# Optimization experiments

Measured on AMD Instinct MI355X. Metric: run time of the kernel, lower is better.

The kernel has to match this reference:

```python
import jax, jax.numpy as jnp
import numpy as np

TEMP = 0.07
BATCH, DIM, NUM_ATTRS = 8192, 512, 4
NUM_PROTOS = 2 ** NUM_ATTRS  # all binary combos present => unique() size is static


def setup_inputs() -> dict:
    key = jax.random.key(0)
    z_flowed = jax.random.normal(key, (BATCH, DIM), dtype=jnp.float32)
    # binary attribute combos, all 16 present; first column = MSB (matches torch.unique row sort)
    combo = jnp.arange(BATCH, dtype=jnp.int32) % NUM_PROTOS
    shifts = jnp.arange(NUM_ATTRS - 1, -1, -1, dtype=jnp.int32)
    attributes = ((combo[:, None] >> shifts[None, :]) & 1).astype(jnp.float32)
    return {"z_flowed": z_flowed, "attributes": attributes}


def _l2norm(x, axis=-1, eps=1e-12):
    n = jnp.sqrt(jnp.sum(x * x, axis=axis, keepdims=True))
    return x / jnp.maximum(n, eps)  # F.normalize semantics


def reference(z_flowed, attributes):
    B, D = z_flowed.shape
    num_attrs = attributes.shape[1]
    P = 2 ** num_attrs
    z_norm = _l2norm(z_flowed, axis=1)

    # inverse indices of torch.unique(attributes, dim=0): binary row -> code (MSB = col 0)
    shifts = jnp.arange(num_attrs - 1, -1, -1)
    inverse = jnp.sum((attributes > 0.5).astype(jnp.int32) * (1 << shifts)[None, :], axis=1)

    # prototype = normalized segment-mean of z_norm per attribute combo (detached)
    sums = jax.ops.segment_sum(z_norm, inverse, num_segments=P)          # [P, D]
    counts = jax.ops.segment_sum(jnp.ones((B,), z_norm.dtype), inverse, num_segments=P)
    means = sums / jnp.maximum(counts, 1.0)[:, None]
    prototypes = jax.lax.stop_gradient(_l2norm(means, axis=1))
    prototypes = jnp.where(counts[:, None] > 0, prototypes, 0.0)

    # prototype contrastive term
    proto_sim = (z_norm @ prototypes.T) / TEMP                            # [B, P]
    exp_sim = jnp.exp(proto_sim)
    pos = exp_sim[jnp.arange(B), inverse]
    alls = jnp.maximum(jnp.sum(exp_sim, axis=1), 1e-8)
    loss = -jnp.mean(jnp.log(pos / alls + 1e-8))

    # pairwise term (positives only when BOTH attribute rows are all-ones)
    pairwise = (z_norm @ z_norm.T) / TEMP                                 # [B, B]
    attr_sim = attributes @ attributes.T
    pos_mask = (attr_sim == num_attrs).astype(z_norm.dtype)
    pos_mask = pos_mask * (1.0 - jnp.eye(B, dtype=z_norm.dtype))
    exp_pw = jnp.exp(pairwise)
    pos_sims = jnp.sum(exp_pw * pos_mask, axis=1)
    all_sims = jnp.sum(exp_pw, axis=1) - jnp.diagonal(exp_pw)
    valid = jnp.sum(pos_mask, axis=1) > 0
    per_row = -jnp.log(pos_sims / (all_sims + 1e-8) + 1e-8)
    n_valid = jnp.sum(valid.astype(z_norm.dtype))
    pairwise_loss = jnp.sum(jnp.where(valid, per_row, 0.0)) / jnp.maximum(n_valid, 1.0)
    loss = jnp.where(n_valid > 0, 0.7 * loss + 0.3 * pairwise_loss, loss)
    return loss
```

## Files before the change

kernel.cpp:

```cpp
#include <hip/hip_runtime.h>
#include <math.h>

#define NB 8192
#define ND 512
#define NPROTO 16
#define NBLK 256
#define TINV 14.285714285714286f
#define PW_BLOCKS 256
#define PL_BLOCKS 256

typedef short short8 __attribute__((ext_vector_type(8)));
typedef float float4v __attribute__((ext_vector_type(4)));

__device__ __forceinline__ unsigned short f2bf(float f) {
  unsigned u = __builtin_bit_cast(unsigned, f);
  unsigned r = (u + 0x7FFFu + ((u >> 16) & 1u)) >> 16;
  return (unsigned short)r;
}
__device__ __forceinline__ float bflo(unsigned u) {
  return __builtin_bit_cast(float, u << 16);
}
__device__ __forceinline__ float bfhi(unsigned u) {
  return __builtin_bit_cast(float, u & 0xFFFF0000u);
}

__global__ __launch_bounds__(512) void k_norm(
    const float* __restrict__ z, const float* __restrict__ attr,
    unsigned short* __restrict__ znb, float* __restrict__ partialSum,
    int* __restrict__ code)
{
  __shared__ float acc[NPROTO * ND];
  const int t = threadIdx.x, lane = t & 63, wid = t >> 6;
  for (int i = t; i < NPROTO * ND; i += 512) acc[i] = 0.f;
  __syncthreads();
  #pragma unroll
  for (int rr = 0; rr < 4; ++rr) {
    const int r = blockIdx.x * 32 + wid * 4 + rr;
    const float* zr = z + (size_t)r * ND;
    float v[8];
    #pragma unroll
    for (int jj = 0; jj < 8; ++jj) v[jj] = zr[lane + jj * 64];
    float s = 0.f;
    #pragma unroll
    for (int jj = 0; jj < 8; ++jj) s += v[jj] * v[jj];
    #pragma unroll
    for (int o = 32; o > 0; o >>= 1) s += __shfl_xor(s, o);
    const float inv = 1.f / fmaxf(sqrtf(s), 1e-12f);
    const float* a = attr + (size_t)r * 4;
    const int c = (a[0] > 0.5f ? 8 : 0) | (a[1] > 0.5f ? 4 : 0) |
                  (a[2] > 0.5f ? 2 : 0) | (a[3] > 0.5f ? 1 : 0);
    float* accRow = acc + c * ND;
    #pragma unroll
    for (int jj = 0; jj < 8; ++jj) {
      const float zv = v[jj] * inv;
      atomicAdd(&accRow[lane + jj * 64], zv);
      znb[(size_t)r * ND + lane + jj * 64] = f2bf(zv);
    }
    if (lane == 0) code[r] = c;
  }
  __syncthreads();
  for (int i = t; i < NPROTO * ND; i += 512) {
    const int p = i >> 9, d = i & 511;
    partialSum[(size_t)((p << 8) | blockIdx.x) * ND + d] = acc[i];
  }
}

__global__ __launch_bounds__(256) void k_reduce1(
    const float* __restrict__ partialSum, float* __restrict__ partial2)
{
  const int t = threadIdx.x;
  const int p = blockIdx.x >> 4, c = blockIdx.x & 15;
  const float* base = partialSum + (size_t)(p * NBLK + c * 16) * ND;
  float s0 = 0.f, s1 = 0.f;
  #pragma unroll
  for (int k = 0; k < 16; ++k) {
    s0 += base[k * ND + t];
    s1 += base[k * ND + t + 256];
  }
  partial2[(size_t)(p * 16 + c) * ND + t] = s0;
  partial2[(size_t)(p * 16 + c) * ND + t + 256] = s1;
}

__global__ __launch_bounds__(512) void k_protonorm(
    const float* __restrict__ partial2, const int* __restrict__ code,
    float* __restrict__ protos, int* __restrict__ validList,
    int* __restrict__ validCnt)
{
  __shared__ float red[8];
  __shared__ int lcnt;
  const int t = threadIdx.x, lane = t & 63, wid = t >> 6;
  const int p = blockIdx.x;
  if (t == 0) lcnt = 0;
  __syncthreads();
  const float* base = partial2 + (size_t)p * 16 * ND;
  float s = 0.f;
  #pragma unroll
  for (int c = 0; c < 16; ++c)
    s += base[c * ND + t];
  float cl = 0.f;
  for (int r = t; r < NB; r += 512) {
    const int match = (code[r] == p) ? 1 : 0;
    cl += (float)match;
    if (p == NPROTO - 1 && match) {
      const int slot = atomicAdd(&lcnt, 1);
      validList[slot] = r;
    }
  }
  #pragma unroll
  for (int o = 32; o > 0; o >>= 1) cl += __shfl_xor(cl, o);
  if (lane == 0) red[wid] = cl;
  __syncthreads();
  const float cTot = red[0]+red[1]+red[2]+red[3]+red[4]+red[5]+red[6]+red[7];
  __syncthreads();
  const float mean = s / fmaxf(cTot, 1.f);
  float sq = mean * mean;
  #pragma unroll
  for (int o = 32; o > 0; o >>= 1) sq += __shfl_xor(sq, o);
  if (lane == 0) red[wid] = sq;
  __syncthreads();
  const float sum = red[0]+red[1]+red[2]+red[3]+red[4]+red[5]+red[6]+red[7];
  const float scale = (cTot > 0.f) ? 1.f / fmaxf(sqrtf(sum), 1e-12f) : 0.f;
  protos[p * ND + t] = mean * scale;
  if (p == NPROTO - 1 && t == 0) validCnt[0] = lcnt;
}

#define PLD (ND + 4)
#define SMEM_BYTES 41472
__global__ __launch_bounds__(512) void k_main(
    const unsigned short* __restrict__ znb, const float* __restrict__ protos,
    const int* __restrict__ code, const int* __restrict__ validList,
    const int* __restrict__ validCnt,
    float* __restrict__ partialAll, float* __restrict__ partialPos,
    float* __restrict__ plPart)
{
  __shared__ __align__(16) char smem[SMEM_BYTES];
  __shared__ float red3[8];
  const int t = threadIdx.x, lane = t & 63, wid = t >> 6;
  const int bi = blockIdx.x;
  if (bi < PW_BLOCKS) {
    unsigned short* aT = (unsigned short*)smem;
    unsigned short* bT = aT + 64 * 64;
    int* rowIdx = (int*)(bT + 256 * 64);
    unsigned char* aoSh = (unsigned char*)(rowIdx + 64);
    const int wv = wid >> 2, ww = wid & 3;
    const int m = validCnt[0];
    const int nIT = (m + 63) >> 6;
    const int items = nIT * 32;
    const int grp = lane >> 4, cl = lane & 15;
    for (int wi = bi; wi < items; wi += PW_BLOCKS) {
      const int i0 = (wi >> 5) * 64;
      const int jt = wi & 31;
      const int jb = jt * 256;
      __syncthreads();
      if (t < 64) rowIdx[t] = (i0 + t < m) ? validList[i0 + t] : -1;
      if (t < 256) aoSh[t] = (code[jb + t] == NPROTO - 1) ? 1 : 0;
      float4v acc[2][4];
      #pragma unroll
      for (int mi = 0; mi < 2; ++mi)
        #pragma unroll
        for (int nj = 0; nj < 4; ++nj) acc[mi][nj] = (float4v)(0.f);
      for (int kc = 0; kc < 8; ++kc) {
        const int k0 = kc * 64;
        __syncthreads();
        {
          const int ia = t >> 3, kq = t & 7;
          const int ri = rowIdx[ia];
          const int srow = (ri < 0) ? 0 : ri;
          const uint4 v = *(const uint4*)(znb + (size_t)srow * ND + k0 + kq * 8);
          *(uint4*)((char*)aT + ia * 128 + ((kq * 16) ^ ((ia & 7) << 4))) = v;
        }
        #pragma unroll
        for (int h = 0; h < 4; ++h) {
          const int f = t + h * 512;
          const int j = f >> 3, kq = f & 7;
          const uint4 v = *(const uint4*)(znb + (size_t)(jb + j) * ND + k0 + kq * 8);
          *(uint4*)((char*)bT + j * 128 + ((kq * 16) ^ ((j & 7) << 4))) = v;
        }
        __syncthreads();
        #pragma unroll
        for (int ks = 0; ks < 2; ++ks) {
          const int kb = ks * 64 + grp * 16;
          short8 af[2], bf[4];
          #pragma unroll
          for (int mi = 0; mi < 2; ++mi) {
            const int rw = wv * 32 + mi * 16 + cl;
            af[mi] = *(const short8*)((char*)aT + rw * 128 + (kb ^ ((rw & 7) << 4)));
          }
          #pragma unroll
          for (int nj = 0; nj < 4; ++nj) {
            const int rw = ww * 64 + nj * 16 + cl;
            bf[nj] = *(const short8*)((char*)bT + rw * 128 + (kb ^ ((rw & 7) << 4)));
          }
          #pragma unroll
          for (int mi = 0; mi < 2; ++mi)
            #pragma unroll
            for (int nj = 0; nj < 4; ++nj)
              acc[mi][nj] = __builtin_amdgcn_mfma_f32_16x16x32_bf16(af[mi], bf[nj], acc[mi][nj], 0, 0, 0);
        }
      }
      #pragma unroll
      for (int mi = 0; mi < 2; ++mi) {
        float sA[4] = {0.f, 0.f, 0.f, 0.f}, sP[4] = {0.f, 0.f, 0.f, 0.f};
        int ri[4];
        #pragma unroll
        for (int q = 0; q < 4; ++q) ri[q] = rowIdx[wv * 32 + mi * 16 + grp * 4 + q];
        #pragma unroll
        for (int nj = 0; nj < 4; ++nj) {
          const int jl = ww * 64 + nj * 16 + cl;
          const int jg = jb + jl;
          const float ao = aoSh[jl] ? 1.f : 0.f;
          #pragma unroll
          for (int q = 0; q < 4; ++q) {
            float e = __expf(acc[mi][nj][q] * TINV);
            e = (jg == ri[q]) ? 0.f : e;
            sA[q] += e;
            sP[q] += e * ao;
          }
        }
        #pragma unroll
        for (int q = 0; q < 4; ++q) {
          #pragma unroll
          for (int o = 1; o < 16; o <<= 1) {
            sA[q] += __shfl_xor(sA[q], o);
            sP[q] += __shfl_xor(sP[q], o);
          }
        }
        if (cl == 0) {
          const int slot0 = i0 + wv * 32 + mi * 16 + grp * 4;
          const int jt2 = jt * 4 + ww;
          if (slot0 + 3 < m) {
            *(float4*)&partialAll[(size_t)jt2 * NB + slot0] =
                make_float4(sA[0], sA[1], sA[2], sA[3]);
            *(float4*)&partialPos[(size_t)jt2 * NB + slot0] =
                make_float4(sP[0], sP[1], sP[2], sP[3]);
          } else {
            #pragma unroll
            for (int q = 0; q < 4; ++q) {
              if (slot0 + q < m) {
                partialAll[(size_t)jt2 * NB + slot0 + q] = sA[q];
                partialPos[(size_t)jt2 * NB + slot0 + q] = sP[q];
              }
            }
          }
        }
      }
    }
  } else {
    float* pl = (float*)smem;
    const int pb = bi - PW_BLOCKS;
    for (int i = t; i < NPROTO * ND; i += 512)
      pl[(i >> 9) * PLD + (i & 511)] = protos[i];
    __syncthreads();
    const int p = lane & 15, grp = lane >> 4;
    float lacc = 0.f;
    #pragma unroll
    for (int rr = 0; rr < 4; ++rr) {
      const int r = pb * 32 + wid * 4 + rr;
      const uint4* zr = (const uint4*)(znb + (size_t)r * ND + grp * 128);
      const float* pbp = &pl[p * PLD + grp * 128];
      float s = 0.f;
      #pragma unroll
      for (int it = 0; it < 16; ++it) {
        const uint4 u = zr[it];
        const float4 p0 = *(const float4*)(pbp + it * 8);
        const float4 p1 = *(const float4*)(pbp + it * 8 + 4);
        s += bflo(u.x)*p0.x + bfhi(u.x)*p0.y + bflo(u.y)*p0.z + bfhi(u.y)*p0.w;
        s += bflo(u.z)*p1.x + bfhi(u.z)*p1.y + bflo(u.w)*p1.z + bfhi(u.w)*p1.w;
      }
      s += __shfl_xor(s, 16);
      s += __shfl_xor(s, 32);
      const float e = __expf(s * TINV);
      float alls = e;
      alls += __shfl_xor(alls, 1);
      alls += __shfl_xor(alls, 2);
      alls += __shfl_xor(alls, 4);
      alls += __shfl_xor(alls, 8);
      const int c = code[r];
      const float pos = __shfl(e, (lane & ~15) | c);
      if (lane == 0) lacc += -logf(pos / fmaxf(alls, 1e-8f) + 1e-8f);
    }
    if (lane == 0) red3[wid] = lacc;
    __syncthreads();
    if (t == 0)
      plPart[pb] = red3[0]+red3[1]+red3[2]+red3[3]+red3[4]+red3[5]+red3[6]+red3[7];
  }
}

__global__ __launch_bounds__(1024) void k_final(
    const float* __restrict__ partialAll, const float* __restrict__ partialPos,
    const float* __restrict__ plPart, const int* __restrict__ validCnt,
    float* __restrict__ out)
{
  __shared__ float shA[1024], shP[1024];
  __shared__ float red[16], red2[16];
  const int t = threadIdx.x, lane = t & 63, wid = t >> 6;
  const int m = validCnt[0];
  const int nvalid = (m >= 2) ? m : 0;
  const int slot = t & 511, half = t >> 9;
  float sa = 0.f, sp = 0.f;
  if (slot < nvalid) {
    const int k0 = half * 64;
    #pragma unroll 8
    for (int k = k0; k < k0 + 64; ++k) {
      sa += partialAll[(size_t)k * NB + slot];
      sp += partialPos[(size_t)k * NB + slot];
    }
  }
  shA[t] = sa; shP[t] = sp;
  __syncthreads();
  float s = 0.f;
  if (t < 512 && slot < nvalid) {
    const float A = shA[t] + shA[t + 512];
    const float P = shP[t] + shP[t + 512];
    s = -logf(P / (A + 1e-8f) + 1e-8f);
  }
  float pls = (t < PL_BLOCKS) ? plPart[t] : 0.f;
  #pragma unroll
  for (int o = 32; o > 0; o >>= 1) {
    s += __shfl_xor(s, o);
    pls += __shfl_xor(pls, o);
  }
  if (lane == 0) { red[wid] = s; red2[wid] = pls; }
  __syncthreads();
  if (t == 0) {
    float total = 0.f, plTot = 0.f;
    #pragma unroll
    for (int w = 0; w < 16; ++w) { total += red[w]; plTot += red2[w]; }
    const float proto = plTot / (float)NB;
    float loss = proto;
    if (nvalid > 0) loss = 0.7f * proto + 0.3f * (total / (float)nvalid);
    out[0] = loss;
  }
}

extern "C" void kernel_launch(void* const* d_in, const int* in_sizes, int n_in,
                              void* d_out, int out_size, void* d_ws, size_t ws_size,
                              hipStream_t stream) {
  const float* z = (const float*)d_in[0];
  const float* attr = (const float*)d_in[1];
  unsigned short* znb = (unsigned short*)d_ws;
  float* partialSum = (float*)(znb + (size_t)NB * ND);
  float* partialAll = partialSum;
  float* partialPos = partialSum + (size_t)128 * NB;
  char* w = (char*)(partialSum + (size_t)NBLK * NPROTO * ND);
  float* partial2 = (float*)w;      w += (size_t)NPROTO * 16 * ND * 4;
  int* validCnt = (int*)w;          w += 16;
  int* code = (int*)w;              w += NB * 4;
  int* validList = (int*)w;         w += NB * 4;
  float* protos = (float*)w;        w += NPROTO * ND * 4;
  float* plPart = (float*)w;        w += PL_BLOCKS * 4;
  k_norm<<<dim3(NBLK), dim3(512), 0, stream>>>(z, attr, znb, partialSum, code);
  k_reduce1<<<dim3(256), dim3(256), 0, stream>>>(partialSum, partial2);
  k_protonorm<<<dim3(NPROTO), dim3(512), 0, stream>>>(partial2, code, protos,
                                                      validList, validCnt);
  k_main<<<dim3(PW_BLOCKS + PL_BLOCKS), dim3(512), 0, stream>>>(
      znb, protos, code, validList, validCnt, partialAll, partialPos, plPart);
  k_final<<<dim3(1), dim3(1024), 0, stream>>>(partialAll, partialPos, plPart,
                                              validCnt, (float*)d_out);
}
```

Baseline: 68.66 us.

## Double-buffer pairwise GEMM tiles using direct global-to-LDS loads

Result: slower. 73.40 us (+6.9%).

```diff
diff --git a/kernel.cpp b/kernel.cpp
--- a/kernel.cpp
+++ b/kernel.cpp
@@ -22,6 +22,11 @@
 }
 __device__ __forceinline__ float bfhi(unsigned u) {
   return __builtin_bit_cast(float, u & 0xFFFF0000u);
+}
+__device__ __forceinline__ void gld16(const unsigned short* g, unsigned short* l) {
+  __builtin_amdgcn_global_load_lds(
+      (const __attribute__((address_space(1))) void*)g,
+      (__attribute__((address_space(3))) void*)l, 16, 0, 0);
 }
 
 __global__ __launch_bounds__(512) void k_norm(
@@ -125,7 +130,7 @@
 }
 
 #define PLD (ND + 4)
-#define SMEM_BYTES 41472
+#define SMEM_BYTES 81920
 __global__ __launch_bounds__(512) void k_main(
     const unsigned short* __restrict__ znb, const float* __restrict__ protos,
     const int* __restrict__ code, const int* __restrict__ validList,
@@ -138,45 +143,57 @@
   const int t = threadIdx.x, lane = t & 63, wid = t >> 6;
   const int bi = blockIdx.x;
   if (bi < PW_BLOCKS) {
-    unsigned short* aT = (unsigned short*)smem;
-    unsigned short* bT = aT + 64 * 64;
-    int* rowIdx = (int*)(bT + 256 * 64);
-    unsigned char* aoSh = (unsigned char*)(rowIdx + 64);
+    char* const Abuf[2] = { smem, smem + 8192 };
+    char* const Bbuf[2] = { smem + 16384, smem + 49152 };
     const int wv = wid >> 2, ww = wid & 3;
     const int m = validCnt[0];
     const int nIT = (m + 63) >> 6;
     const int items = nIT * 32;
     const int grp = lane >> 4, cl = lane & 15;
+    const int iaA = t >> 3;
+    const int kqA = (t & 7) ^ (iaA & 7);
     for (int wi = bi; wi < items; wi += PW_BLOCKS) {
       const int i0 = (wi >> 5) * 64;
       const int jt = wi & 31;
       const int jb = jt * 256;
-      __syncthreads();
-      if (t < 64) rowIdx[t] = (i0 + t < m) ? validList[i0 + t] : -1;
-      if (t < 256) aoSh[t] = (code[jb + t] == NPROTO - 1) ? 1 : 0;
+      const int slotA = i0 + iaA;
+      const int srowA = (slotA < m) ? validList[slotA] : 0;
+      {
+        gld16(znb + (size_t)srowA * ND + kqA * 8,
+              (unsigned short*)(Abuf[0] + wid * 1024));
+        #pragma unroll
+        for (int h = 0; h < 4; ++h) {
+          const int ci = h * 512 + t;
+          const int j = ci >> 3;
+          const int kq = (t & 7) ^ (j & 7);
+          gld16(znb + (size_t)(jb + j) * ND + kq * 8,
+                (unsigned short*)(Bbuf[0] + h * 8192 + wid * 1024));
+        }
+      }
       float4v acc[2][4];
       #pragma unroll
       for (int mi = 0; mi < 2; ++mi)
         #pragma unroll
         for (int nj = 0; nj < 4; ++nj) acc[mi][nj] = (float4v)(0.f);
+      int cur = 0;
+      #pragma unroll
       for (int kc = 0; kc < 8; ++kc) {
-        const int k0 = kc * 64;
         __syncthreads();
-        {
-          const int ia = t >> 3, kq = t & 7;
-          const int ri = rowIdx[ia];
-          const int srow = (ri < 0) ? 0 : ri;
-          const uint4 v = *(const uint4*)(znb + (size_t)srow * ND + k0 + kq * 8);
-          *(uint4*)((char*)aT + ia * 128 + ((kq * 16) ^ ((ia & 7) << 4))) = v;
-        }
-        #pragma unroll
-        for (int h = 0; h < 4; ++h) {
-          const int f = t + h * 512;
-          const int j = f >> 3, kq = f & 7;
-          const uint4 v = *(const uint4*)(znb + (size_t)(jb + j) * ND + k0 + kq * 8);
-          *(uint4*)((char*)bT + j * 128 + ((kq * 16) ^ ((j & 7) << 4))) = v;
-        }
-        __syncthreads();
+        if (kc < 7) {
+          const int k0 = (kc + 1) * 64;
+          gld16(znb + (size_t)srowA * ND + k0 + kqA * 8,
+                (unsigned short*)(Abuf[cur ^ 1] + wid * 1024));
+          #pragma unroll
+          for (int h = 0; h < 4; ++h) {
+            const int ci = h * 512 + t;
+            const int j = ci >> 3;
+            const int kq = (t & 7) ^ (j & 7);
+            gld16(znb + (size_t)(jb + j) * ND + k0 + kq * 8,
+                  (unsigned short*)(Bbuf[cur ^ 1] + h * 8192 + wid * 1024));
+          }
+        }
+        const char* aC = Abuf[cur];
+        const char* bC = Bbuf[cur];
         #pragma unroll
         for (int ks = 0; ks < 2; ++ks) {
           const int kb = ks * 64 + grp * 16;
@@ -184,12 +201,12 @@
           #pragma unroll
           for (int mi = 0; mi < 2; ++mi) {
             const int rw = wv * 32 + mi * 16 + cl;
-            af[mi] = *(const short8*)((char*)aT + rw * 128 + (kb ^ ((rw & 7) << 4)));
+            af[mi] = *(const short8*)(aC + rw * 128 + (kb ^ ((rw & 7) << 4)));
           }
           #pragma unroll
           for (int nj = 0; nj < 4; ++nj) {
             const int rw = ww * 64 + nj * 16 + cl;
-            bf[nj] = *(const short8*)((char*)bT + rw * 128 + (kb ^ ((rw & 7) << 4)));
+            bf[nj] = *(const short8*)(bC + rw * 128 + (kb ^ ((rw & 7) << 4)));
           }
           #pragma unroll
           for (int mi = 0; mi < 2; ++mi)
@@ -197,18 +214,22 @@
             for (int nj = 0; nj < 4; ++nj)
               acc[mi][nj] = __builtin_amdgcn_mfma_f32_16x16x32_bf16(af[mi], bf[nj], acc[mi][nj], 0, 0, 0);
         }
+        cur ^= 1;
       }
       #pragma unroll
       for (int mi = 0; mi < 2; ++mi) {
         float sA[4] = {0.f, 0.f, 0.f, 0.f}, sP[4] = {0.f, 0.f, 0.f, 0.f};
         int ri[4];
         #pragma unroll
-        for (int q = 0; q < 4; ++q) ri[q] = rowIdx[wv * 32 + mi * 16 + grp * 4 + q];
+        for (int q = 0; q < 4; ++q) {
+          const int sl = i0 + wv * 32 + mi * 16 + grp * 4 + q;
+          ri[q] = (sl < m) ? validList[sl] : -1;
+        }
         #pragma unroll
         for (int nj = 0; nj < 4; ++nj) {
           const int jl = ww * 64 + nj * 16 + cl;
           const int jg = jb + jl;
-          const float ao = aoSh[jl] ? 1.f : 0.f;
+          const float ao = (code[jg] == NPROTO - 1) ? 1.f : 0.f;
           #pragma unroll
           for (int q = 0; q < 4; ++q) {
             float e = __expf(acc[mi][nj][q] * TINV);
```

## Merge prototype reduction into atomics and fold normalization into main kernel

Applied to the files above, without the earlier changes.

After: 72.05 us. 4.9% more time.

```diff
diff --git a/kernel.cpp b/kernel.cpp
--- a/kernel.cpp
+++ b/kernel.cpp
@@ -27,11 +27,13 @@
 __global__ __launch_bounds__(512) void k_norm(
     const float* __restrict__ z, const float* __restrict__ attr,
     unsigned short* __restrict__ znb, float* __restrict__ partialSum,
-    int* __restrict__ code)
+    int* __restrict__ code, float* __restrict__ protoSumG)
 {
   __shared__ float acc[NPROTO * ND];
   const int t = threadIdx.x, lane = t & 63, wid = t >> 6;
   for (int i = t; i < NPROTO * ND; i += 512) acc[i] = 0.f;
+  if (blockIdx.x == 0)
+    for (int i = t; i < NPROTO * ND; i += 512) protoSumG[i] = 0.f;
   __syncthreads();
   #pragma unroll
   for (int rr = 0; rr < 4; ++rr) {
@@ -66,68 +68,41 @@
 }
 
 __global__ __launch_bounds__(256) void k_reduce1(
-    const float* __restrict__ partialSum, float* __restrict__ partial2)
+    const float* __restrict__ partialSum, const int* __restrict__ code,
+    float* __restrict__ protoSumG, int* __restrict__ validList,
+    int* __restrict__ validCnt)
 {
   const int t = threadIdx.x;
-  const int p = blockIdx.x >> 4, c = blockIdx.x & 15;
-  const float* base = partialSum + (size_t)(p * NBLK + c * 16) * ND;
-  float s0 = 0.f, s1 = 0.f;
-  #pragma unroll
-  for (int k = 0; k < 16; ++k) {
-    s0 += base[k * ND + t];
-    s1 += base[k * ND + t + 256];
-  }
-  partial2[(size_t)(p * 16 + c) * ND + t] = s0;
-  partial2[(size_t)(p * 16 + c) * ND + t + 256] = s1;
-}
-
-__global__ __launch_bounds__(512) void k_protonorm(
-    const float* __restrict__ partial2, const int* __restrict__ code,
-    float* __restrict__ protos, int* __restrict__ validList,
-    int* __restrict__ validCnt)
-{
-  __shared__ float red[8];
-  __shared__ int lcnt;
-  const int t = threadIdx.x, lane = t & 63, wid = t >> 6;
-  const int p = blockIdx.x;
-  if (t == 0) lcnt = 0;
-  __syncthreads();
-  const float* base = partial2 + (size_t)p * 16 * ND;
-  float s = 0.f;
-  #pragma unroll
-  for (int c = 0; c < 16; ++c)
-    s += base[c * ND + t];
-  float cl = 0.f;
-  for (int r = t; r < NB; r += 512) {
-    const int match = (code[r] == p) ? 1 : 0;
-    cl += (float)match;
-    if (p == NPROTO - 1 && match) {
-      const int slot = atomicAdd(&lcnt, 1);
-      validList[slot] = r;
-    }
-  }
-  #pragma unroll
-  for (int o = 32; o > 0; o >>= 1) cl += __shfl_xor(cl, o);
-  if (lane == 0) red[wid] = cl;
-  __syncthreads();
-  const float cTot = red[0]+red[1]+red[2]+red[3]+red[4]+red[5]+red[6]+red[7];
-  __syncthreads();
-  const float mean = s / fmaxf(cTot, 1.f);
-  float sq = mean * mean;
-  #pragma unroll
-  for (int o = 32; o > 0; o >>= 1) sq += __shfl_xor(sq, o);
-  if (lane == 0) red[wid] = sq;
-  __syncthreads();
-  const float sum = red[0]+red[1]+red[2]+red[3]+red[4]+red[5]+red[6]+red[7];
-  const float scale = (cTot > 0.f) ? 1.f / fmaxf(sqrtf(sum), 1e-12f) : 0.f;
-  protos[p * ND + t] = mean * scale;
-  if (p == NPROTO - 1 && t == 0) validCnt[0] = lcnt;
+  if (blockIdx.x < 256) {
+    const int p = blockIdx.x >> 4, c = blockIdx.x & 15;
+    const float* base = partialSum + (size_t)(p * NBLK + c * 16) * ND;
+    float s0 = 0.f, s1 = 0.f;
+    #pragma unroll
+    for (int k = 0; k < 16; ++k) {
+      s0 += base[k * ND + t];
+      s1 += base[k * ND + t + 256];
+    }
+    atomicAdd(&protoSumG[p * ND + t], s0);
+    atomicAdd(&protoSumG[p * ND + t + 256], s1);
+  } else {
+    __shared__ int lcnt;
+    if (t == 0) lcnt = 0;
+    __syncthreads();
+    for (int r = t; r < NB; r += 256) {
+      if (code[r] == NPROTO - 1) {
+        const int s = atomicAdd(&lcnt, 1);
+        validList[s] = r;
+      }
+    }
+    __syncthreads();
+    if (t == 0) validCnt[0] = lcnt;
+  }
 }
 
 #define PLD (ND + 4)
 #define SMEM_BYTES 41472
 __global__ __launch_bounds__(512) void k_main(
-    const unsigned short* __restrict__ znb, const float* __restrict__ protos,
+    const unsigned short* __restrict__ znb, const float* __restrict__ protoSumG,
     const int* __restrict__ code, const int* __restrict__ validList,
     const int* __restrict__ validCnt,
     float* __restrict__ partialAll, float* __restrict__ partialPos,
@@ -135,6 +110,7 @@
 {
   __shared__ __align__(16) char smem[SMEM_BYTES];
   __shared__ float red3[8];
+  __shared__ float gSh[16];
   const int t = threadIdx.x, lane = t & 63, wid = t >> 6;
   const int bi = blockIdx.x;
   if (bi < PW_BLOCKS) {
@@ -249,7 +225,23 @@
     float* pl = (float*)smem;
     const int pb = bi - PW_BLOCKS;
     for (int i = t; i < NPROTO * ND; i += 512)
-      pl[(i >> 9) * PLD + (i & 511)] = protos[i];
+      pl[(i >> 9) * PLD + (i & 511)] = protoSumG[i];
+    __syncthreads();
+    {
+      const int p = t >> 5, l32 = t & 31;
+      float sq = 0.f;
+      #pragma unroll
+      for (int k = 0; k < 16; ++k) {
+        const float v = pl[p * PLD + l32 + k * 32];
+        sq += v * v;
+      }
+      #pragma unroll
+      for (int o = 1; o < 32; o <<= 1) sq += __shfl_xor(sq, o);
+      if (l32 == 0) gSh[p] = 1.f / fmaxf(sqrtf(sq), 1e-12f);
+    }
+    __syncthreads();
+    for (int i = t; i < NPROTO * ND; i += 512)
+      pl[(i >> 9) * PLD + (i & 511)] *= gSh[i >> 9];
     __syncthreads();
     const int p = lane & 15, grp = lane >> 4;
     float lacc = 0.f;
@@ -343,18 +335,17 @@
   float* partialAll = partialSum;
   float* partialPos = partialSum + (size_t)128 * NB;
   char* w = (char*)(partialSum + (size_t)NBLK * NPROTO * ND);
-  float* partial2 = (float*)w;      w += (size_t)NPROTO * 16 * ND * 4;
+  float* protoSumG = (float*)w;     w += NPROTO * ND * 4;
   int* validCnt = (int*)w;          w += 16;
   int* code = (int*)w;              w += NB * 4;
   int* validList = (int*)w;         w += NB * 4;
-  float* protos = (float*)w;        w += NPROTO * ND * 4;
   float* plPart = (float*)w;        w += PL_BLOCKS * 4;
-  k_norm<<<dim3(NBLK), dim3(512), 0, stream>>>(z, attr, znb, partialSum, code);
-  k_reduce1<<<dim3(256), dim3(256), 0, stream>>>(partialSum, partial2);
-  k_protonorm<<<dim3(NPROTO), dim3(512), 0, stream>>>(partial2, code, protos,
-                                                      validList, validCnt);
+  k_norm<<<dim3(NBLK), dim3(512), 0, stream>>>(z, attr, znb, partialSum, code,
+                                               protoSumG);
+  k_reduce1<<<dim3(257), dim3(256), 0, stream>>>(partialSum, code, protoSumG,
+                                                 validList, validCnt);
   k_main<<<dim3(PW_BLOCKS + PL_BLOCKS), dim3(512), 0, stream>>>(
-      znb, protos, code, validList, validCnt, partialAll, partialPos, plPart);
+      znb, protoSumG, code, validList, validCnt, partialAll, partialPos, plPart);
   k_final<<<dim3(1), dim3(1024), 0, stream>>>(partialAll, partialPos, plPart,
                                               validCnt, (float*)d_out);
 }
```
